# Optimization experiments

Measured on AMD Instinct MI355X. Metric: run time of the kernel, lower is better.

The kernel has to match this reference:

```python
import jax, jax.numpy as jnp
import numpy as np

N, E, M = 100000, 1600000, 1000
DIN = DZ = DOUT = 128


def setup_inputs() -> dict:
    key = jax.random.key(0)
    ks = jax.random.split(key, 7)
    x = jax.random.normal(ks[0], (N, DIN), dtype=jnp.float32)
    edge_index = jax.random.randint(ks[1], (2, E), 0, N, dtype=jnp.int32)
    bc_feature = jax.random.normal(ks[2], (M, DZ), dtype=jnp.float32)
    bc_assignment = jax.random.randint(ks[3], (N,), 0, M, dtype=jnp.int32)
    s = 1.0 / np.sqrt(DIN)
    WX = jax.random.uniform(ks[4], (DIN, DOUT), jnp.float32, -s, s)
    WZ = jax.random.uniform(ks[5], (DZ, DOUT), jnp.float32, -s, s)
    Walpha = jax.random.uniform(ks[6], (DZ, DOUT), jnp.float32, -s, s)
    return {"x": x, "edge_index": edge_index, "bc_feature": bc_feature,
            "bc_assignment": bc_assignment, "WX": WX, "WZ": WZ, "Walpha": Walpha}


def reference(x, edge_index, bc_feature, bc_assignment, WX, WZ, Walpha):
    n, m = x.shape[0], bc_feature.shape[0]
    row, col = edge_index[0], edge_index[1]

    # Ahat = D (I + A) D, D = diag(colsum(I+A))^-1/2 (duplicate edges sum, as in coalesce)
    deg = 1.0 + jax.ops.segment_sum(jnp.ones_like(col, jnp.float32), col, num_segments=n)
    d = deg ** -0.5  # [n]

    def ahat_mm(H):  # H: [n, D] -> Ahat @ H, without materializing n x n
        msg = d[col][:, None] * H[col]                      # [E, D]
        agg = jax.ops.segment_sum(msg, row, num_segments=n)  # neighbor part
        return d[:, None] * (agg + d[:, None] * H)           # self-loop part d_i^2 H_i

    # Bhat = Drow (eye(n,m) + B) Dcol; B[i, assign[i]] = 1, m <= n
    cnt = jax.ops.segment_sum(jnp.ones((n,), jnp.float32), bc_assignment, num_segments=m)
    dcol = (1.0 + cnt) ** -0.5                               # eye adds 1 per column (m <= n)
    rowsum = 1.0 + (jnp.arange(n) < m).astype(jnp.float32)   # eye diag only for i < m
    drow = rowsum ** -0.5

    def bhat_mm(H):  # H: [m, D] -> Bhat @ H : [n, D]
        out = dcol[bc_assignment][:, None] * H[bc_assignment]  # assignment edge term
        out = out.at[:m].add(dcol[:, None] * H)                # rectangular-eye term
        return drow[:, None] * out

    Xprime = ahat_mm(x @ WX)
    Zprime = bhat_mm(bc_feature @ WZ)
    Zalpha = ahat_mm(bhat_mm(bc_feature @ Walpha))
    return (Xprime + Zprime + Zalpha) / 3.0  # mean-fuse of the three sources
```

## Files before the change

### kernel.cpp

```cpp
#include <hip/hip_runtime.h>

#define RSQRT2 0.70710678118654752f

typedef unsigned int uint;
typedef unsigned char uchar;

#define MAXNB 512
#define EPB   4096

__device__ __forceinline__ uint pack_bf16x2(float a, float b) {
    uint ua = __float_as_uint(a), ub = __float_as_uint(b);
    ua += 0x7FFFu + ((ua >> 16) & 1u);
    ub += 0x7FFFu + ((ub >> 16) & 1u);
    return (ua >> 16) | (ub & 0xFFFF0000u);
}
__device__ __forceinline__ float blo(uint g) { return __uint_as_float(g << 16); }
__device__ __forceinline__ float bhi(uint g) { return __uint_as_float(g & 0xFFFF0000u); }


__global__ __launch_bounds__(256) void k_coarse(
    const int* __restrict__ ei, int E,
    const int* __restrict__ assign, int N, int NB,
    int* __restrict__ coarse_row, int* __restrict__ coarse_col,
    int* __restrict__ bc_cnt) {
    __shared__ int lr[MAXNB], lc[MAXNB];
    int t = threadIdx.x;
    for (int i = t; i < NB; i += 256) { lr[i] = 0; lc[i] = 0; }
    __syncthreads();
    int base = blockIdx.x * EPB;
#pragma unroll
    for (int k = 0; k < 16; ++k) {
        int e = base + t + k * 256;
        if (e < E) {
            atomicAdd(&lr[ei[e] >> 8], 1);
            atomicAdd(&lc[ei[E + e] >> 8], 1);
        }
    }
    int i = blockIdx.x * 256 + t;
    if (i < N) atomicAdd(&bc_cnt[assign[i]], 1);
    __syncthreads();
    for (int b = t; b < NB; b += 256) {
        if (lr[b]) atomicAdd(&coarse_row[b], lr[b]);
        if (lc[b]) atomicAdd(&coarse_col[b], lc[b]);
    }
}


__global__ __launch_bounds__(1024) void k_scan_small(
    const int* __restrict__ coarse_row, const int* __restrict__ coarse_col,
    const int* __restrict__ bc_cnt, int NB, int M, int E, int N,
    int* __restrict__ row_off, int* __restrict__ col_off,
    float* __restrict__ dcol, int* __restrict__ row_ptr) {
    __shared__ int sm[1024];
    int t = threadIdx.x;
    int half = t >> 9;
    int lt = t & 511;
    int v = (lt < NB) ? (half ? coarse_col[lt] : coarse_row[lt]) : 0;
    sm[t] = v;
    __syncthreads();
    for (int off = 1; off < 512; off <<= 1) {
        int u = (lt >= off) ? sm[t - off] : 0;
        __syncthreads();
        sm[t] += u;
        __syncthreads();
    }
    if (lt <= NB) (half ? col_off : row_off)[lt] = sm[t] - v;
    for (int i = t; i < M; i += 1024) dcol[i] = rsqrtf(1.0f + (float)bc_cnt[i]);
    if (t == 0) row_ptr[N] = E;
}


__global__ __launch_bounds__(256) void k_scatter(
    const int* __restrict__ ei, int E, int NB,
    const int* __restrict__ row_off, const int* __restrict__ col_off,
    int* __restrict__ fill_row, int* __restrict__ fill_col,
    uint* __restrict__ packed, uchar* __restrict__ colb) {
    __shared__ int lr[MAXNB], lc[MAXNB], rbase[MAXNB], cbase[MAXNB];
    int t = threadIdx.x;
    for (int i = t; i < NB; i += 256) { lr[i] = 0; lc[i] = 0; }
    __syncthreads();
    int base = blockIdx.x * EPB;
#pragma unroll
    for (int k = 0; k < 16; ++k) {
        int e = base + t + k * 256;
        if (e < E) {
            atomicAdd(&lr[ei[e] >> 8], 1);
            atomicAdd(&lc[ei[E + e] >> 8], 1);
        }
    }
    __syncthreads();
    for (int b = t; b < NB; b += 256) {
        int cr = lr[b];
        if (cr) rbase[b] = row_off[b] + atomicAdd(&fill_row[b], cr);
        lr[b] = 0;
        int cc = lc[b];
        if (cc) cbase[b] = col_off[b] + atomicAdd(&fill_col[b], cc);
        lc[b] = 0;
    }
    __syncthreads();
#pragma unroll
    for (int k = 0; k < 16; ++k) {
        int e = base + t + k * 256;
        if (e < E) {
            int r = ei[e], c = ei[E + e];
            int rb = r >> 8, cb = c >> 8;
            int pr = atomicAdd(&lr[rb], 1);
            packed[rbase[rb] + pr] = ((uint)(r & 255) << 24) | (uint)c;
            int pc = atomicAdd(&lc[cb], 1);
            colb[cbase[cb] + pc] = (uchar)(c & 255);
        }
    }
}


__global__ __launch_bounds__(256) void k_fine_row(
    const uint* __restrict__ packed, const int* __restrict__ row_off,
    int N, int* __restrict__ row_ptr, int* __restrict__ col_sorted) {
    __shared__ int h[256], cur[256];
    int t = threadIdx.x, b = blockIdx.x;
    int s = row_off[b], e = row_off[b + 1];
    h[t] = 0;
    __syncthreads();
    for (int j = s + t; j < e; j += 256) atomicAdd(&h[packed[j] >> 24], 1);
    __syncthreads();
    int v = h[t];
    for (int off = 1; off < 256; off <<= 1) {
        int u = (t >= off) ? h[t - off] : 0;
        __syncthreads();
        h[t] += u;
        __syncthreads();
    }
    int excl = h[t] - v;
    cur[t] = excl;
    int gr = b * 256 + t;
    if (gr < N) row_ptr[gr] = s + excl;
    __syncthreads();
    for (int j = s + t; j < e; j += 256) {
        uint p = packed[j];
        int pos = atomicAdd(&cur[p >> 24], 1);
        col_sorted[s + pos] = (int)(p & 0xFFFFFFu);
    }
}


__global__ __launch_bounds__(256) void k_fine_col(
    const uchar* __restrict__ colb, const int* __restrict__ col_off,
    int N, float* __restrict__ d) {
    __shared__ int h[256];
    int t = threadIdx.x, b = blockIdx.x;
    int s = col_off[b], e = col_off[b + 1];
    h[t] = 0;
    __syncthreads();
    for (int j = s + t; j < e; j += 256) atomicAdd(&h[colb[j]], 1);
    __syncthreads();
    int gc = b * 256 + t;
    if (gc < N) d[gc] = rsqrtf(1.0f + (float)h[t]);
}


__global__ __launch_bounds__(128) void k_bc_gemm(
    const float* __restrict__ bcf, const float* __restrict__ WZ,
    const float* __restrict__ WA, float* __restrict__ ZW, float* __restrict__ ZA, int M) {
    __shared__ float rows[16][128];
    int c = threadIdx.x;
    int r0 = blockIdx.x * 16;
    int nr = M - r0; if (nr > 16) nr = 16;
    for (int idx = c; idx < nr * 128; idx += 128)
        rows[idx >> 7][idx & 127] = bcf[r0 * 128 + idx];
    __syncthreads();
    float aW[16], aA[16];
#pragma unroll
    for (int r = 0; r < 16; ++r) { aW[r] = 0.f; aA[r] = 0.f; }
#pragma unroll 4
    for (int k = 0; k < 128; ++k) {
        float wz = WZ[k * 128 + c];
        float wa = WA[k * 128 + c];
#pragma unroll
        for (int r = 0; r < 16; ++r) {
            float xv = rows[r][k];
            aW[r] = fmaf(xv, wz, aW[r]);
            aA[r] = fmaf(xv, wa, aA[r]);
        }
    }
    for (int r = 0; r < nr; ++r) {
        ZW[(r0 + r) * 128 + c] = aW[r];
        ZA[(r0 + r) * 128 + c] = aA[r];
    }
}


#define GB_ROWS 64
#define GB_KC 64

__global__ __launch_bounds__(256) void k_G(
    const float* __restrict__ x, const float* __restrict__ WX,
    const float* __restrict__ ZA, const int* __restrict__ assign,
    const float* __restrict__ dcol, uint* __restrict__ Gp, int N, int M) {
    __shared__ float xs[GB_ROWS][GB_KC + 1];
    __shared__ float ws[GB_KC][128];

    int tid = threadIdx.x;
    int tc = tid & 15;
    int tr = tid >> 4;
    int row0 = blockIdx.x * GB_ROWS;
    int c0 = tc * 8;

    float acc[4][8];
#pragma unroll
    for (int r = 0; r < 4; ++r)
#pragma unroll
        for (int j = 0; j < 8; ++j) acc[r][j] = 0.f;

    bool full = (row0 + GB_ROWS <= N);

    for (int kc = 0; kc < 128; kc += GB_KC) {
        if (full) {
#pragma unroll
            for (int it = 0; it < 4; ++it) {
                int idx = tid + 256 * it;
                int r = idx >> 4, k4 = (idx & 15) * 4;
                float4 v = *(const float4*)&x[(size_t)(row0 + r) * 128 + kc + k4];
                xs[r][k4] = v.x; xs[r][k4 + 1] = v.y; xs[r][k4 + 2] = v.z; xs[r][k4 + 3] = v.w;
            }
        } else {
            for (int idx = tid; idx < GB_ROWS * GB_KC; idx += 256) {
                int r = idx >> 6, k = idx & 63;
                int gr = row0 + r;
                xs[r][k] = (gr < N) ? x[(size_t)gr * 128 + kc + k] : 0.f;
            }
        }
#pragma unroll
        for (int it = 0; it < 8; ++it) {
            int idx = tid + 256 * it;
            int k = idx >> 5, c4 = (idx & 31) * 4;
            float4 v = *(const float4*)&WX[(size_t)(kc + k) * 128 + c4];
            ws[k][c4] = v.x; ws[k][c4 + 1] = v.y; ws[k][c4 + 2] = v.z; ws[k][c4 + 3] = v.w;
        }
        __syncthreads();
#pragma unroll 4
        for (int k = 0; k < GB_KC; ++k) {
            float a0 = xs[tr * 4 + 0][k];
            float a1 = xs[tr * 4 + 1][k];
            float a2 = xs[tr * 4 + 2][k];
            float a3 = xs[tr * 4 + 3][k];
            float4 b0 = *(const float4*)&ws[k][c0];
            float4 b1 = *(const float4*)&ws[k][c0 + 4];
            float bv[8] = {b0.x, b0.y, b0.z, b0.w, b1.x, b1.y, b1.z, b1.w};
#pragma unroll
            for (int j = 0; j < 8; ++j) {
                float b = bv[j];
                acc[0][j] = fmaf(a0, b, acc[0][j]);
                acc[1][j] = fmaf(a1, b, acc[1][j]);
                acc[2][j] = fmaf(a2, b, acc[2][j]);
                acc[3][j] = fmaf(a3, b, acc[3][j]);
            }
        }
        __syncthreads();
    }

#pragma unroll
    for (int rr = 0; rr < 4; ++rr) {
        int gr = row0 + tr * 4 + rr;
        if (gr >= N) continue;
        int ai = assign[gr];
        float dca = dcol[ai];
        float dr = (gr < M) ? RSQRT2 : 1.0f;
        float dci = (gr < M) ? dcol[gr] : 0.0f;
        float v[8];
#pragma unroll
        for (int j = 0; j < 8; ++j) {
            float bh = dca * ZA[ai * 128 + c0 + j];
            if (gr < M) bh = fmaf(dci, ZA[gr * 128 + c0 + j], bh);
            v[j] = acc[rr][j] + bh * dr;
        }
        uint4 w;
        w.x = pack_bf16x2(v[0], v[1]);
        w.y = pack_bf16x2(v[2], v[3]);
        w.z = pack_bf16x2(v[4], v[5]);
        w.w = pack_bf16x2(v[6], v[7]);
        *(uint4*)&Gp[(size_t)gr * 64 + (c0 >> 1)] = w;
    }
}


__global__ __launch_bounds__(256) void k_final(
    const uint* __restrict__ Gp, const float* __restrict__ d,
    const int* __restrict__ row_ptr, const int* __restrict__ col_sorted,
    const float* __restrict__ ZW, const float* __restrict__ dcol,
    const int* __restrict__ assign, float* __restrict__ out, int N, int M) {
    int wid = threadIdx.x >> 6;
    int lane = threadIdx.x & 63;
    int i = blockIdx.x * 4 + wid;
    if (i >= N) return;

    int s = row_ptr[i];
    int e = row_ptr[i + 1];
    float ax = 0.f, ay = 0.f;
    int j = s;
    for (; j + 4 <= e; j += 4) {
        int c0 = col_sorted[j];
        int c1 = col_sorted[j + 1];
        int c2 = col_sorted[j + 2];
        int c3 = col_sorted[j + 3];
        uint g0 = Gp[(size_t)c0 * 64 + lane];
        uint g1 = Gp[(size_t)c1 * 64 + lane];
        uint g2 = Gp[(size_t)c2 * 64 + lane];
        uint g3 = Gp[(size_t)c3 * 64 + lane];
        float d0 = d[c0], d1 = d[c1], d2 = d[c2], d3 = d[c3];
        ax = fmaf(d0, blo(g0), ax); ay = fmaf(d0, bhi(g0), ay);
        ax = fmaf(d1, blo(g1), ax); ay = fmaf(d1, bhi(g1), ay);
        ax = fmaf(d2, blo(g2), ax); ay = fmaf(d2, bhi(g2), ay);
        ax = fmaf(d3, blo(g3), ax); ay = fmaf(d3, bhi(g3), ay);
    }
    for (; j < e; ++j) {
        int c = col_sorted[j];
        uint g = Gp[(size_t)c * 64 + lane];
        float dc = d[c];
        ax = fmaf(dc, blo(g), ax);
        ay = fmaf(dc, bhi(g), ay);
    }
    float di = d[i];
    uint gi = Gp[(size_t)i * 64 + lane];
    float ox = di * fmaf(di, blo(gi), ax);
    float oy = di * fmaf(di, bhi(gi), ay);

    int ai = assign[i];
    float dca = dcol[ai];
    const float2* ZW2 = (const float2*)ZW;
    float2 zw = ZW2[ai * 64 + lane];
    float zx = dca * zw.x, zy = dca * zw.y;
    if (i < M) {
        float dci = dcol[i];
        float2 zwi = ZW2[i * 64 + lane];
        zx = fmaf(dci, zwi.x, zx);
        zy = fmaf(dci, zwi.y, zy);
    }
    float dr = (i < M) ? RSQRT2 : 1.0f;

    float2 o;
    o.x = (ox + zx * dr) * (1.0f / 3.0f);
    o.y = (oy + zy * dr) * (1.0f / 3.0f);
    ((float2*)out)[(size_t)i * 64 + lane] = o;
}


extern "C" void kernel_launch(void* const* d_in, const int* in_sizes, int n_in,
                              void* d_out, int out_size, void* d_ws, size_t ws_size,
                              hipStream_t stream) {
    const float* x      = (const float*)d_in[0];
    const int*   ei     = (const int*)d_in[1];
    const float* bcf    = (const float*)d_in[2];
    const int*   assign = (const int*)d_in[3];
    const float* WX     = (const float*)d_in[4];
    const float* WZ     = (const float*)d_in[5];
    const float* WA     = (const float*)d_in[6];
    float* out = (float*)d_out;

    const int N = in_sizes[0] / 128;
    const int E = in_sizes[1] / 2;
    const int M = in_sizes[2] / 128;
    const int NB = (N + 255) >> 8;

    char* p = (char*)d_ws;
    auto alloc = [&](size_t bytes) -> void* {
        void* r = (void*)p;
        p += (bytes + 255) & ~(size_t)255;
        return r;
    };
    int*   coarse_row = (int*)alloc(MAXNB * 4);
    int*   coarse_col = (int*)alloc(MAXNB * 4);
    int*   fill_row   = (int*)alloc(MAXNB * 4);
    int*   fill_col   = (int*)alloc(MAXNB * 4);
    int*   bc_cnt     = (int*)alloc((size_t)M * 4);
    size_t zero_bytes = (size_t)(p - (char*)d_ws);
    int*   row_off    = (int*)alloc((MAXNB + 1) * 4);
    int*   col_off    = (int*)alloc((MAXNB + 1) * 4);
    int*   row_ptr    = (int*)alloc((size_t)(N + 1) * 4);
    float* dvec       = (float*)alloc((size_t)N * 4);
    float* dcol       = (float*)alloc((size_t)M * 4);
    float* ZW         = (float*)alloc((size_t)M * 128 * 4);
    float* ZA         = (float*)alloc((size_t)M * 128 * 4);
    uint*  packed     = (uint*)alloc((size_t)E * 4);
    uchar* colb       = (uchar*)alloc((size_t)E);
    int*   col_sorted = (int*)alloc((size_t)E * 4);
    uint*  Gp         = (uint*)alloc((size_t)N * 64 * 4);

    hipMemsetAsync(d_ws, 0, zero_bytes, stream);

    int nbE = (E + EPB - 1) / EPB;
    int nbN = (N + 255) / 256;
    int nbK1 = nbE > nbN ? nbE : nbN;

    k_coarse<<<nbK1, 256, 0, stream>>>(ei, E, assign, N, NB, coarse_row, coarse_col, bc_cnt);
    k_bc_gemm<<<(M + 15) / 16, 128, 0, stream>>>(bcf, WZ, WA, ZW, ZA, M);
    k_scan_small<<<1, 1024, 0, stream>>>(coarse_row, coarse_col, bc_cnt, NB, M, E, N,
                                         row_off, col_off, dcol, row_ptr);
    k_scatter<<<nbE, 256, 0, stream>>>(ei, E, NB, row_off, col_off,
                                       fill_row, fill_col, packed, colb);
    k_fine_row<<<NB, 256, 0, stream>>>(packed, row_off, N, row_ptr, col_sorted);
    k_fine_col<<<NB, 256, 0, stream>>>(colb, col_off, N, dvec);

    k_G<<<(N + GB_ROWS - 1) / GB_ROWS, 256, 0, stream>>>(x, WX, ZA, assign, dcol, Gp, N, M);
    k_final<<<(N + 3) / 4, 256, 0, stream>>>(Gp, dvec, row_ptr, col_sorted, ZW, dcol, assign, out, N, M);
}
```

Measured before the change: 356.3 us.

## Use bf16 MFMA for X·WX and prescale G rows by degree norm

Replaces the shared-memory FP32 FMA tile GEMM in k_G with bf16 MFMA 16x16x32 instructions. Operands are converted to bf16 in registers and each wave computes 32 rows. The per-source-node d[c] factor is folded into G when it is written, so the gather in k_final drops the d[] loads and FMAs and becomes plain adds, unrolled 8 deep. This cuts GEMM compute and per-edge random loads, at the cost of extra bf16 rounding of x and WX inputs and uncoalesced per-element stores of G using shuffles.

```diff
diff --git a/kernel.cpp b/kernel.cpp
--- a/kernel.cpp
+++ b/kernel.cpp
@@ -4,6 +4,8 @@
 
 typedef unsigned int uint;
 typedef unsigned char uchar;
+typedef __attribute__((ext_vector_type(8))) short bf16x8;
+typedef __attribute__((ext_vector_type(4))) float f32x4;
 
 #define MAXNB 512
 #define EPB   4096
@@ -189,96 +191,85 @@
 }
 
 
-#define GB_ROWS 64
-#define GB_KC 64
-
 __global__ __launch_bounds__(256) void k_G(
     const float* __restrict__ x, const float* __restrict__ WX,
     const float* __restrict__ ZA, const int* __restrict__ assign,
-    const float* __restrict__ dcol, uint* __restrict__ Gp, int N, int M) {
-    __shared__ float xs[GB_ROWS][GB_KC + 1];
-    __shared__ float ws[GB_KC][128];
-
-    int tid = threadIdx.x;
-    int tc = tid & 15;
-    int tr = tid >> 4;
-    int row0 = blockIdx.x * GB_ROWS;
-    int c0 = tc * 8;
-
-    float acc[4][8];
-#pragma unroll
-    for (int r = 0; r < 4; ++r)
-#pragma unroll
-        for (int j = 0; j < 8; ++j) acc[r][j] = 0.f;
-
-    bool full = (row0 + GB_ROWS <= N);
-
-    for (int kc = 0; kc < 128; kc += GB_KC) {
-        if (full) {
-#pragma unroll
-            for (int it = 0; it < 4; ++it) {
-                int idx = tid + 256 * it;
-                int r = idx >> 4, k4 = (idx & 15) * 4;
-                float4 v = *(const float4*)&x[(size_t)(row0 + r) * 128 + kc + k4];
-                xs[r][k4] = v.x; xs[r][k4 + 1] = v.y; xs[r][k4 + 2] = v.z; xs[r][k4 + 3] = v.w;
+    const float* __restrict__ dcol, const float* __restrict__ dvec,
+    uint* __restrict__ Gp, int N, int M) {
+    int lane = threadIdx.x & 63;
+    int wid = threadIdx.x >> 6;
+    int r0 = blockIdx.x * 128 + wid * 32;
+    int lrow = lane & 15;
+    int lg = lane >> 4;
+
+    f32x4 acc[2][8];
+#pragma unroll
+    for (int rt = 0; rt < 2; ++rt)
+#pragma unroll
+        for (int ct = 0; ct < 8; ++ct) acc[rt][ct] = (f32x4){0.f, 0.f, 0.f, 0.f};
+
+    union BU { uint u[4]; bf16x8 v; };
+
+    for (int kt = 0; kt < 4; ++kt) {
+        int kb = kt * 32 + lg * 8;
+        BU B[8];
+#pragma unroll
+        for (int ct = 0; ct < 8; ++ct) {
+            float b0 = WX[(size_t)(kb + 0) * 128 + ct * 16 + lrow];
+            float b1 = WX[(size_t)(kb + 1) * 128 + ct * 16 + lrow];
+            float b2 = WX[(size_t)(kb + 2) * 128 + ct * 16 + lrow];
+            float b3 = WX[(size_t)(kb + 3) * 128 + ct * 16 + lrow];
+            float b4 = WX[(size_t)(kb + 4) * 128 + ct * 16 + lrow];
+            float b5 = WX[(size_t)(kb + 5) * 128 + ct * 16 + lrow];
+            float b6 = WX[(size_t)(kb + 6) * 128 + ct * 16 + lrow];
+            float b7 = WX[(size_t)(kb + 7) * 128 + ct * 16 + lrow];
+            B[ct].u[0] = pack_bf16x2(b0, b1);
+            B[ct].u[1] = pack_bf16x2(b2, b3);
+            B[ct].u[2] = pack_bf16x2(b4, b5);
+            B[ct].u[3] = pack_bf16x2(b6, b7);
+        }
+#pragma unroll
+        for (int rt = 0; rt < 2; ++rt) {
+            int ar = r0 + rt * 16 + lrow;
+            int arc = ar < N ? ar : N - 1;
+            const float* xp = &x[(size_t)arc * 128 + kb];
+            float4 a0 = *(const float4*)xp;
+            float4 a1 = *(const float4*)(xp + 4);
+            BU A;
+            A.u[0] = pack_bf16x2(a0.x, a0.y);
+            A.u[1] = pack_bf16x2(a0.z, a0.w);
+            A.u[2] = pack_bf16x2(a1.x, a1.y);
+            A.u[3] = pack_bf16x2(a1.z, a1.w);
+#pragma unroll
+            for (int ct = 0; ct < 8; ++ct)
+                acc[rt][ct] = __builtin_amdgcn_mfma_f32_16x16x32_bf16(
+                    A.v, B[ct].v, acc[rt][ct], 0, 0, 0);
+        }
+    }
+
+#pragma unroll
+    for (int rt = 0; rt < 2; ++rt) {
+#pragma unroll
+        for (int r = 0; r < 4; ++r) {
+            int srow = r0 + rt * 16 + lg * 4 + r;
+            int sc = srow < N ? srow : N - 1;
+            float dn = dvec[sc];
+            int ai = assign[sc];
+            float dca = dcol[ai];
+            bool im = (sc < M);
+            float drw = im ? RSQRT2 : 1.0f;
+            float dci = im ? dcol[sc] : 0.0f;
+#pragma unroll
+            for (int ct = 0; ct < 8; ++ct) {
+                int col = ct * 16 + lrow;
+                float bh = dca * ZA[(size_t)ai * 128 + col];
+                if (im) bh = fmaf(dci, ZA[(size_t)sc * 128 + col], bh);
+                float v = dn * (acc[rt][ct][r] + bh * drw);
+                float vpartner = __shfl_xor(v, 1);
+                if (((lane & 1) == 0) && srow < N)
+                    Gp[(size_t)srow * 64 + ct * 8 + (lrow >> 1)] = pack_bf16x2(v, vpartner);
             }
-        } else {
-            for (int idx = tid; idx < GB_ROWS * GB_KC; idx += 256) {
-                int r = idx >> 6, k = idx & 63;
-                int gr = row0 + r;
-                xs[r][k] = (gr < N) ? x[(size_t)gr * 128 + kc + k] : 0.f;
-            }
-        }
-#pragma unroll
-        for (int it = 0; it < 8; ++it) {
-            int idx = tid + 256 * it;
-            int k = idx >> 5, c4 = (idx & 31) * 4;
-            float4 v = *(const float4*)&WX[(size_t)(kc + k) * 128 + c4];
-            ws[k][c4] = v.x; ws[k][c4 + 1] = v.y; ws[k][c4 + 2] = v.z; ws[k][c4 + 3] = v.w;
-        }
-        __syncthreads();
-#pragma unroll 4
-        for (int k = 0; k < GB_KC; ++k) {
-            float a0 = xs[tr * 4 + 0][k];
-            float a1 = xs[tr * 4 + 1][k];
-            float a2 = xs[tr * 4 + 2][k];
-            float a3 = xs[tr * 4 + 3][k];
-            float4 b0 = *(const float4*)&ws[k][c0];
-            float4 b1 = *(const float4*)&ws[k][c0 + 4];
-            float bv[8] = {b0.x, b0.y, b0.z, b0.w, b1.x, b1.y, b1.z, b1.w};
-#pragma unroll
-            for (int j = 0; j < 8; ++j) {
-                float b = bv[j];
-                acc[0][j] = fmaf(a0, b, acc[0][j]);
-                acc[1][j] = fmaf(a1, b, acc[1][j]);
-                acc[2][j] = fmaf(a2, b, acc[2][j]);
-                acc[3][j] = fmaf(a3, b, acc[3][j]);
-            }
-        }
-        __syncthreads();
-    }
-
-#pragma unroll
-    for (int rr = 0; rr < 4; ++rr) {
-        int gr = row0 + tr * 4 + rr;
-        if (gr >= N) continue;
-        int ai = assign[gr];
-        float dca = dcol[ai];
-        float dr = (gr < M) ? RSQRT2 : 1.0f;
-        float dci = (gr < M) ? dcol[gr] : 0.0f;
-        float v[8];
-#pragma unroll
-        for (int j = 0; j < 8; ++j) {
-            float bh = dca * ZA[ai * 128 + c0 + j];
-            if (gr < M) bh = fmaf(dci, ZA[gr * 128 + c0 + j], bh);
-            v[j] = acc[rr][j] + bh * dr;
-        }
-        uint4 w;
-        w.x = pack_bf16x2(v[0], v[1]);
-        w.y = pack_bf16x2(v[2], v[3]);
-        w.z = pack_bf16x2(v[4], v[5]);
-        w.w = pack_bf16x2(v[6], v[7]);
-        *(uint4*)&Gp[(size_t)gr * 64 + (c0 >> 1)] = w;
+        }
     }
 }
 
@@ -297,32 +288,31 @@
     int e = row_ptr[i + 1];
     float ax = 0.f, ay = 0.f;
     int j = s;
-    for (; j + 4 <= e; j += 4) {
-        int c0 = col_sorted[j];
-        int c1 = col_sorted[j + 1];
-        int c2 = col_sorted[j + 2];
-        int c3 = col_sorted[j + 3];
+    for (; j + 8 <= e; j += 8) {
+        int c0 = col_sorted[j],     c1 = col_sorted[j + 1];
+        int c2 = col_sorted[j + 2], c3 = col_sorted[j + 3];
+        int c4 = col_sorted[j + 4], c5 = col_sorted[j + 5];
+        int c6 = col_sorted[j + 6], c7 = col_sorted[j + 7];
         uint g0 = Gp[(size_t)c0 * 64 + lane];
         uint g1 = Gp[(size_t)c1 * 64 + lane];
         uint g2 = Gp[(size_t)c2 * 64 + lane];
         uint g3 = Gp[(size_t)c3 * 64 + lane];
-        float d0 = d[c0], d1 = d[c1], d2 = d[c2], d3 = d[c3];
-        ax = fmaf(d0, blo(g0), ax); ay = fmaf(d0, bhi(g0), ay);
-        ax = fmaf(d1, blo(g1), ax); ay = fmaf(d1, bhi(g1), ay);
-        ax = fmaf(d2, blo(g2), ax); ay = fmaf(d2, bhi(g2), ay);
-        ax = fmaf(d3, blo(g3), ax); ay = fmaf(d3, bhi(g3), ay);
+        uint g4 = Gp[(size_t)c4 * 64 + lane];
+        uint g5 = Gp[(size_t)c5 * 64 + lane];
+        uint g6 = Gp[(size_t)c6 * 64 + lane];
+        uint g7 = Gp[(size_t)c7 * 64 + lane];
+        ax += blo(g0) + blo(g1) + blo(g2) + blo(g3) + blo(g4) + blo(g5) + blo(g6) + blo(g7);
+        ay += bhi(g0) + bhi(g1) + bhi(g2) + bhi(g3) + bhi(g4) + bhi(g5) + bhi(g6) + bhi(g7);
     }
     for (; j < e; ++j) {
-        int c = col_sorted[j];
-        uint g = Gp[(size_t)c * 64 + lane];
-        float dc = d[c];
-        ax = fmaf(dc, blo(g), ax);
-        ay = fmaf(dc, bhi(g), ay);
+        uint g = Gp[(size_t)col_sorted[j] * 64 + lane];
+        ax += blo(g);
+        ay += bhi(g);
     }
     float di = d[i];
     uint gi = Gp[(size_t)i * 64 + lane];
-    float ox = di * fmaf(di, blo(gi), ax);
-    float oy = di * fmaf(di, bhi(gi), ay);
+    float ox = di * (ax + blo(gi));
+    float oy = di * (ay + bhi(gi));
 
     int ai = assign[i];
     float dca = dcol[ai];
@@ -400,6 +390,6 @@
     k_fine_row<<<NB, 256, 0, stream>>>(packed, row_off, N, row_ptr, col_sorted);
     k_fine_col<<<NB, 256, 0, stream>>>(colb, col_off, N, dvec);
 
-    k_G<<<(N + GB_ROWS - 1) / GB_ROWS, 256, 0, stream>>>(x, WX, ZA, assign, dcol, Gp, N, M);
+    k_G<<<(N + 127) / 128, 256, 0, stream>>>(x, WX, ZA, assign, dcol, dvec, Gp, N, M);
     k_final<<<(N + 3) / 4, 256, 0, stream>>>(Gp, dvec, row_ptr, col_sorted, ZW, dcol, assign, out, N, M);
 }
```

Result: faster. 348.9 us (-2.1%).
